# Performance work log

Measured on AMD Instinct MI355X. Metric: run time of the kernel, lower is better.

Reference implementation:

```python
import jax, jax.numpy as jnp
import numpy as np

B, D_IN, D_FEAT, N_EX, N_LAB = 4096, 512, 512, 20000, 100
P_FACTOR = 3.0
EPS = 1e-12  # torch F.normalize eps


def setup_inputs() -> dict:
    key = jax.random.key(0)
    k1, k2, k3, k4 = jax.random.split(key, 4)
    features = jax.random.normal(k1, (B, D_IN), dtype=jnp.float32)
    g_weight = jax.random.normal(k2, (D_FEAT, D_IN), dtype=jnp.float32) * (1.0 / np.sqrt(D_IN))
    ex_features = jax.random.normal(k3, (N_EX, D_IN), dtype=jnp.float32)
    ex_classes = jax.random.uniform(k4, (N_EX, N_LAB), dtype=jnp.float32)
    class_reps = jnp.eye(N_LAB, dtype=jnp.float32)  # one_hot(arange(num_labels)) since class_dim is None
    return {"features": features, "g_weight": g_weight, "ex_features": ex_features,
            "ex_classes": ex_classes, "class_reps": class_reps}


def _l2_normalize(x):
    n = jnp.linalg.norm(x, axis=-1, keepdims=True)
    return x / jnp.maximum(n, EPS)


def _l1_normalize(x):
    n = jnp.sum(jnp.abs(x), axis=-1, keepdims=True)
    return x / jnp.maximum(n, EPS)


def reference(features, g_weight, ex_features, ex_classes, class_reps):
    # g projection (bias-free linear)
    f = features @ g_weight.T          # [B, D_FEAT]
    e = ex_features @ g_weight.T       # [N_EX, D_FEAT]
    # exemplar class representations
    ex_class_reps = _l1_normalize(ex_classes) @ class_reps  # [N_EX, N_LAB]
    # cosine similarity
    s = _l2_normalize(f) @ _l2_normalize(e).T  # [B, N_EX]
    # power-sign activation then L1 row-normalize
    a = jnp.sign(s) * jnp.abs(s) ** P_FACTOR
    a = _l1_normalize(a)
    echo = a @ ex_class_reps           # [B, N_LAB]
    return echo
```

## Files before the change

### kernel.cpp

```cpp
#include <hip/hip_runtime.h>

#define B_ROWS 4096
#define D      512
#define N_EX   20000
#define EXP2   20096
#define N_LAB  100
#define LABP2  128
#define NT2    157
#define SPLITS 16

typedef __attribute__((ext_vector_type(8)))  short short8v;
typedef __attribute__((ext_vector_type(4)))  short short4v;
typedef __attribute__((ext_vector_type(4)))  float f32x4;
typedef __attribute__((ext_vector_type(16))) float f32x16;
typedef __attribute__((ext_vector_type(2)))  int   int2v;
typedef unsigned short u16;

__device__ __forceinline__ u16 f2bf(float x) {
    unsigned u = __builtin_bit_cast(unsigned, x);
    u = u + 0x7FFFu + ((u >> 16) & 1u);
    return (u16)(u >> 16);
}
__device__ __forceinline__ float bf2f(u16 h) {
    unsigned u = ((unsigned)h) << 16;
    return __builtin_bit_cast(float, u);
}

__device__ __forceinline__ float wave_reduce_sum(float v) {
    #pragma unroll
    for (int off = 32; off > 0; off >>= 1) v += __shfl_down(v, off, 64);
    return v;
}

__device__ __forceinline__ void gload16(const void* g, void* l) {
    __builtin_amdgcn_global_load_lds((const __attribute__((address_space(1))) void*)g,
                                     (__attribute__((address_space(3))) void*)l, 16, 0, 0);
}

__device__ __forceinline__ unsigned pk_bf16(float a, float b) {
    unsigned r;
    asm("v_cvt_pk_bf16_f32 %0, %1, %2" : "=v"(r) : "v"(a), "v"(b));
    return r;
}

__device__ __forceinline__ void swap_halves(unsigned &a, unsigned &b) {
#if __has_builtin(__builtin_amdgcn_permlane32_swap)
    int2v r = __builtin_amdgcn_permlane32_swap((int)a, (int)b, false, false);
    a = (unsigned)r[0]; b = (unsigned)r[1];
#else
    unsigned sa = (unsigned)__shfl_xor((int)a, 32, 64);
    unsigned sb = (unsigned)__shfl_xor((int)b, 32, 64);
    if (threadIdx.x & 32) a = sb; else b = sa;
#endif
}

#define MFMA16(a, b, c) __builtin_amdgcn_mfma_f32_16x16x32_bf16((a), (b), (c), 0, 0, 0)
#define MFMA32(a, b, c) __builtin_amdgcn_mfma_f32_32x32x16_bf16((a), (b), (c), 0, 0, 0)

__global__ __launch_bounds__(256, 2)
void proj_k(const float* __restrict__ X, const float* __restrict__ W,
            u16* __restrict__ Chi, int M) {
    __shared__ u16 AH[64][72], AL[64][72], BH[64][72];
    const int tid = threadIdx.x;
    const int lane = tid & 63, wave = tid >> 6;
    const int wm = wave >> 1, wn = wave & 1;
    const int l15 = lane & 15, l4 = lane >> 4;
    const int m0 = blockIdx.x * 64, n0 = blockIdx.y * 64;
    f32x4 acc[2][2] = {};
    for (int kc = 0; kc < 8; ++kc) {
        __syncthreads();
        #pragma unroll
        for (int s = 0; s < 2; ++s) {
            int ix = tid + s * 256;
            int r = ix >> 3, c = ix & 7;
            float va[8] = {0.f,0.f,0.f,0.f,0.f,0.f,0.f,0.f};
            if (m0 + r < M) {
                const float* p = &X[(size_t)(m0 + r) * D + kc * 64 + c * 8];
                float4 t0 = *(const float4*)p, t1 = *(const float4*)(p + 4);
                va[0]=t0.x; va[1]=t0.y; va[2]=t0.z; va[3]=t0.w;
                va[4]=t1.x; va[5]=t1.y; va[6]=t1.z; va[7]=t1.w;
            }
            short8v h, l;
            #pragma unroll
            for (int j = 0; j < 8; ++j) {
                u16 hh = f2bf(va[j]); h[j] = (short)hh; l[j] = (short)f2bf(va[j] - bf2f(hh));
            }
            *(short8v*)&AH[r][c*8] = h; *(short8v*)&AL[r][c*8] = l;
            const float* q = &W[(size_t)(n0 + r) * D + kc * 64 + c * 8];
            float4 s0 = *(const float4*)q, s1 = *(const float4*)(q + 4);
            float vb[8] = {s0.x,s0.y,s0.z,s0.w,s1.x,s1.y,s1.z,s1.w};
            #pragma unroll
            for (int j = 0; j < 8; ++j) h[j] = (short)f2bf(vb[j]);
            *(short8v*)&BH[r][c*8] = h;
        }
        __syncthreads();
        #pragma unroll
        for (int ks = 0; ks < 2; ++ks) {
            const int ko = ks * 32 + l4 * 8;
            short8v ah0 = *(const short8v*)&AH[wm*32      + l15][ko];
            short8v ah1 = *(const short8v*)&AH[wm*32 + 16 + l15][ko];
            short8v al0 = *(const short8v*)&AL[wm*32      + l15][ko];
            short8v al1 = *(const short8v*)&AL[wm*32 + 16 + l15][ko];
            short8v bh0 = *(const short8v*)&BH[wn*32      + l15][ko];
            short8v bh1 = *(const short8v*)&BH[wn*32 + 16 + l15][ko];
            acc[0][0] = MFMA16(ah0, bh0, acc[0][0]); acc[0][0] = MFMA16(al0, bh0, acc[0][0]);
            acc[0][1] = MFMA16(ah0, bh1, acc[0][1]); acc[0][1] = MFMA16(al0, bh1, acc[0][1]);
            acc[1][0] = MFMA16(ah1, bh0, acc[1][0]); acc[1][0] = MFMA16(al1, bh0, acc[1][0]);
            acc[1][1] = MFMA16(ah1, bh1, acc[1][1]); acc[1][1] = MFMA16(al1, bh1, acc[1][1]);
        }
    }
    #pragma unroll
    for (int mi = 0; mi < 2; ++mi)
      #pragma unroll
      for (int ni = 0; ni < 2; ++ni)
        #pragma unroll
        for (int r = 0; r < 4; ++r) {
            int row = m0 + wm*32 + mi*16 + l4*4 + r;
            int col = n0 + wn*32 + ni*16 + l15;
            Chi[(size_t)row * D + col] = f2bf(acc[mi][ni][r]);
        }
}

__global__ __launch_bounds__(128)
void l2norm_k(u16* __restrict__ hi) {
    const int row = blockIdx.x, tid = threadIdx.x;
    const size_t base = (size_t)row * D + tid * 4;
    short4v hv = *(short4v*)&hi[base];
    float v[4]; float ss = 0.f;
    #pragma unroll
    for (int j = 0; j < 4; ++j) { v[j] = bf2f((u16)hv[j]); ss += v[j] * v[j]; }
    ss = wave_reduce_sum(ss);
    __shared__ float red[2];
    if ((tid & 63) == 0) red[tid >> 6] = ss;
    __syncthreads();
    float inv = 1.0f / fmaxf(sqrtf(red[0] + red[1]), 1e-12f);
    short4v ho;
    #pragma unroll
    for (int j = 0; j < 4; ++j) ho[j] = (short)f2bf(v[j] * inv);
    *(short4v*)&hi[base] = ho;
}

__global__ __launch_bounds__(256)
void ecrT_k(const float* __restrict__ exc, const float* __restrict__ creps,
            u16* __restrict__ th) {
    __shared__ float CRT[N_LAB][101];
    __shared__ float EX[128][N_LAB];
    __shared__ float INV[128];
    __shared__ u16 OUT[LABP2][128];
    const int tid = threadIdx.x;
    const int e0 = blockIdx.x * 128;
    for (int i = tid; i < N_LAB * N_LAB; i += 256) {
        int c = i / N_LAB, lab = i % N_LAB;
        CRT[lab][c] = creps[i];
    }
    for (int i = tid; i < 128 * N_LAB; i += 256) {
        int el = i / N_LAB, c = i % N_LAB;
        int e = e0 + el;
        EX[el][c] = (e < N_EX) ? exc[(size_t)e * N_LAB + c] : 0.f;
    }
    __syncthreads();
    if (tid < 128) {
        float s = 0.f;
        for (int c = 0; c < N_LAB; ++c) s += fabsf(EX[tid][c]);
        INV[tid] = 1.0f / fmaxf(s, 1e-12f);
    }
    __syncthreads();
    const int lab = tid & 127;
    for (int el = tid >> 7; el < 128; el += 2) {
        float acc = 0.f;
        if (lab < N_LAB) {
            #pragma unroll 4
            for (int c = 0; c < N_LAB; ++c) acc += EX[el][c] * CRT[lab][c];
            acc *= INV[el];
        }
        OUT[lab][el] = f2bf(acc);
    }
    __syncthreads();
    for (int i = tid; i < LABP2 * 16; i += 256) {
        int lb = i >> 4, ch = i & 15;
        *(short8v*)&th[(size_t)lb * EXP2 + e0 + ch * 8] = *(const short8v*)&OUT[lb][ch * 8];
    }
}

__global__ __launch_bounds__(512, 4)
void fused_k(const u16* __restrict__ fnh, const u16* __restrict__ enh,
             const u16* __restrict__ ecth,
             float* __restrict__ nump, float* __restrict__ denp2) {
    __shared__ u16 SM[2][128][64];
    __shared__ u16 WT[LABP2][128];

    const int tid = threadIdx.x;
    const int l = tid & 63, w = tid >> 6;
    const int we = w >> 2, wq = w & 3;
    const int l31 = l & 31, l5 = l >> 5;
    const int m0 = blockIdx.x * 128;
    const int split = blockIdx.y;
    const int r_in = l >> 3;
    const int c16s = (l & 7) ^ r_in;

    union FragU { short8v s; unsigned u[4]; };

    f32x16 num_acc[4] = {};
    float den_th = 0.f;

    for (int t = split; t < NT2; t += SPLITS) {
        const int e0 = t * 128;
        f32x16 sacc[2] = {};
        for (int kc = 0; kc < 8; ++kc) {
            __syncthreads();
            const int kofs = kc * 64;
            #pragma unroll
            for (int i = 0; i < 2; ++i) {
                const int q = w * 2 + i;
                const int row = q * 8 + r_in;
                gload16(&enh[(size_t)(e0 + row) * D + kofs + c16s * 8],
                        (u16*)&SM[0][0][0] + q * 512);
                gload16(&fnh[(size_t)(m0 + row) * D + kofs + c16s * 8],
                        (u16*)&SM[1][0][0] + q * 512);
            }
            if (kc == 7) {
                #pragma unroll
                for (int p = 0; p < 4; ++p) {
                    const int row = p * 32 + w * 4 + (l >> 4);
                    const int ch = l & 15;
                    gload16(&ecth[(size_t)row * EXP2 + e0 + ((ch ^ (row & 7)) * 8)],
                            &WT[0][0] + (p * 32 + w * 4) * 128);
                }
            }
            __syncthreads();
            #pragma unroll
            for (int ks = 0; ks < 4; ++ks) {
                short8v aE[2], bF;
                #pragma unroll
                for (int ei = 0; ei < 2; ++ei) {
                    int row = we * 64 + ei * 32 + l31;
                    int cc = ((ks * 2 + l5) ^ (row & 7)) * 8;
                    aE[ei] = *(const short8v*)((const u16*)&SM[0][0][0] + row * 64 + cc);
                }
                {
                    int row = wq * 32 + l31;
                    int cc = ((ks * 2 + l5) ^ (row & 7)) * 8;
                    bF = *(const short8v*)((const u16*)&SM[1][0][0] + row * 64 + cc);
                }
                sacc[0] = MFMA32(aE[0], bF, sacc[0]);
                sacc[1] = MFMA32(aE[1], bF, sacc[1]);
            }
        }
        #pragma unroll
        for (int ei = 0; ei < 2; ++ei) {
            float a3[16];
            #pragma unroll
            for (int r = 0; r < 16; ++r) {
                float sv = sacc[ei][r];
                float c3 = sv * sv * sv;
                a3[r] = c3;
                den_th += fabsf(c3);
            }
            FragU fr[2];
            #pragma unroll
            for (int c = 0; c < 2; ++c) {
                unsigned p01 = pk_bf16(a3[c*8+0], a3[c*8+1]);
                unsigned p23 = pk_bf16(a3[c*8+2], a3[c*8+3]);
                unsigned p45 = pk_bf16(a3[c*8+4], a3[c*8+5]);
                unsigned p67 = pk_bf16(a3[c*8+6], a3[c*8+7]);
                swap_halves(p01, p45);
                swap_halves(p23, p67);
                fr[c].u[0] = p01; fr[c].u[1] = p23; fr[c].u[2] = p45; fr[c].u[3] = p67;
            }
            #pragma unroll
            for (int c = 0; c < 2; ++c) {
                const int kch = we * 4 + ei * 2 + c;
                #pragma unroll
                for (int lt = 0; lt < 4; ++lt) {
                    int row = lt * 32 + l31;
                    int cc = ((kch * 2 + l5) ^ (row & 7)) * 8;
                    short8v wf = *(const short8v*)(&WT[0][0] + row * 128 + cc);
                    num_acc[lt] = MFMA32(fr[c].s, wf, num_acc[lt]);
                }
            }
        }
    }

    {
        float v = den_th;
        v += __shfl_xor(v, 32, 64);
        if (l5 == 0)
            denp2[((size_t)split * 2 + we) * B_ROWS + m0 + wq * 32 + l31] = v;
    }

    float* SMf = (float*)&SM[0][0][0];
    __syncthreads();
    #pragma unroll
    for (int half = 0; half < 2; ++half) {
        if (we == 1 && (wq >> 1) == half) {
            #pragma unroll
            for (int lt = 0; lt < 4; ++lt)
                #pragma unroll
                for (int r = 0; r < 16; ++r) {
                    int rowf = (r & 3) + 8 * (r >> 2) + 4 * l5;
                    SMf[((wq & 1) * 32 + rowf) * 128 + lt * 32 + l31] = num_acc[lt][r];
                }
        }
        __syncthreads();
        if (we == 0 && (wq >> 1) == half) {
            #pragma unroll
            for (int lt = 0; lt < 4; ++lt)
                #pragma unroll
                for (int r = 0; r < 16; ++r) {
                    int rowf = (r & 3) + 8 * (r >> 2) + 4 * l5;
                    float v = num_acc[lt][r] + SMf[((wq & 1) * 32 + rowf) * 128 + lt * 32 + l31];
                    int m = m0 + wq * 32 + rowf;
                    nump[((size_t)split * B_ROWS + m) * LABP2 + lt * 32 + l31] = v;
                }
        }
        __syncthreads();
    }
}

__global__ __launch_bounds__(128)
void finalize_k(const float* __restrict__ nump, const float* __restrict__ denp2,
                float* __restrict__ out) {
    const int row = blockIdx.x, tid = threadIdx.x;
    float den = 0.f;
    for (int s = 0; s < 2 * SPLITS; ++s)
        den += denp2[(size_t)s * B_ROWS + row];
    if (tid < N_LAB) {
        float acc = 0.f;
        for (int s = 0; s < SPLITS; ++s)
            acc += nump[((size_t)s * B_ROWS + row) * LABP2 + tid];
        out[(size_t)row * N_LAB + tid] = acc / fmaxf(den, 1e-12f);
    }
}

extern "C" void kernel_launch(void* const* d_in, const int* in_sizes, int n_in,
                              void* d_out, int out_size, void* d_ws, size_t ws_size,
                              hipStream_t stream) {
    (void)in_sizes; (void)n_in; (void)out_size; (void)ws_size;
    const float* features    = (const float*)d_in[0];
    const float* g_weight    = (const float*)d_in[1];
    const float* ex_features = (const float*)d_in[2];
    const float* ex_classes  = (const float*)d_in[3];
    const float* class_reps  = (const float*)d_in[4];
    float* out = (float*)d_out;

    size_t off = 0;
    auto alloc = [&](size_t bytes) {
        void* p = (char*)d_ws + off;
        off += (bytes + 255) & ~(size_t)255;
        return p;
    };
    u16* fnh = (u16*)alloc((size_t)B_ROWS * D * 2);
    u16* enh = (u16*)alloc((size_t)EXP2 * D * 2);
    u16* ecth = (u16*)alloc((size_t)LABP2 * EXP2 * 2);
    float* nump  = (float*)alloc((size_t)SPLITS * B_ROWS * LABP2 * 4);
    float* denp2 = (float*)alloc((size_t)2 * SPLITS * B_ROWS * 4);

    proj_k<<<dim3(B_ROWS / 64, 8), 256, 0, stream>>>(features, g_weight, fnh, B_ROWS);
    proj_k<<<dim3(EXP2 / 64, 8), 256, 0, stream>>>(ex_features, g_weight, enh, N_EX);
    l2norm_k<<<B_ROWS, 128, 0, stream>>>(fnh);
    l2norm_k<<<EXP2, 128, 0, stream>>>(enh);
    ecrT_k<<<NT2, 256, 0, stream>>>(ex_classes, class_reps, ecth);
    fused_k<<<dim3(B_ROWS / 128, SPLITS), 512, 0, stream>>>(fnh, enh, ecth, nump, denp2);
    finalize_k<<<B_ROWS, 128, 0, stream>>>(nump, denp2, out);
}
```

Before: 420.2 us.

## Double-buffer fused similarity kernel and project exemplars via bf16 GEMM

The fused similarity kernel now uses a double-buffered 128x128 LDS tile. It prefetches the next k-chunk, the class-weight tile, or the next tile's first chunk while MFMAs run on the current buffer, which removes one barrier per iteration. The exemplar projection moves from the hi/lo split proj_k path to a plain bf16 conversion followed by a single-pass 128x128 MFMA GEMM, with the nump workspace reused as scratch. This aims to hide global load latency and cut projection cost, at some cost in precision for the exemplar features.

```diff
diff --git a/kernel.cpp b/kernel.cpp
--- a/kernel.cpp
+++ b/kernel.cpp
@@ -56,6 +56,87 @@
 
 #define MFMA16(a, b, c) __builtin_amdgcn_mfma_f32_16x16x32_bf16((a), (b), (c), 0, 0, 0)
 #define MFMA32(a, b, c) __builtin_amdgcn_mfma_f32_32x32x16_bf16((a), (b), (c), 0, 0, 0)
+
+__global__ __launch_bounds__(256)
+void splitH_k(const float* __restrict__ src, u16* __restrict__ dst,
+              int src_rows, int dst_rows) {
+    int i8 = blockIdx.x * 256 + threadIdx.x;
+    if (i8 >= dst_rows * 64) return;
+    int row = i8 >> 6;
+    int e = (i8 & 63) * 8;
+    short8v h = {0,0,0,0,0,0,0,0};
+    if (row < src_rows) {
+        const float* p = &src[(size_t)row * D + e];
+        float4 a = *(const float4*)p, b = *(const float4*)(p + 4);
+        float v[8] = {a.x,a.y,a.z,a.w,b.x,b.y,b.z,b.w};
+        #pragma unroll
+        for (int j = 0; j < 8; ++j) h[j] = (short)f2bf(v[j]);
+    }
+    *(short8v*)&dst[(size_t)row * D + e] = h;
+}
+
+__global__ __launch_bounds__(512, 4)
+void gemm128_k(const u16* __restrict__ A, const u16* __restrict__ B,
+               u16* __restrict__ C) {
+    __shared__ u16 BUF[2][128][128];
+    const int tid = threadIdx.x;
+    const int l = tid & 63, w = tid >> 6;
+    const int wa = w >> 2, wb = w & 3;
+    const int l31 = l & 31, l5 = l >> 5;
+    const int m0 = blockIdx.x * 128, n0 = blockIdx.y * 128;
+    const int qrow_in = l >> 4;
+    const int gs = l & 15;
+
+    f32x16 sacc[2] = {};
+
+    auto STAGE = [&](int nx, int kc_) {
+        const int kofs = kc_ * 64;
+        #pragma unroll
+        for (int i = 0; i < 4; ++i) {
+            const int q = w * 4 + i;
+            const int r = q * 4 + qrow_in;
+            const int g = gs ^ (r & 15);
+            const u16* src = (g < 8)
+                ? &A[(size_t)(m0 + r) * D + kofs + g * 8]
+                : &B[(size_t)(n0 + r) * D + kofs + (g - 8) * 8];
+            gload16(src, (u16*)&BUF[nx][0][0] + q * 512);
+        }
+    };
+
+    STAGE(0, 0);
+    __syncthreads();
+    int cur = 0;
+    for (int kc = 0; kc < 8; ++kc) {
+        if (kc < 7) STAGE(cur ^ 1, kc + 1);
+        const u16* base = &BUF[cur][0][0];
+        #pragma unroll
+        for (int ks = 0; ks < 4; ++ks) {
+            const int gk = ks * 2 + l5;
+            short8v aX[2], bW;
+            #pragma unroll
+            for (int ei = 0; ei < 2; ++ei) {
+                int r = wa * 64 + ei * 32 + l31;
+                aX[ei] = *(const short8v*)(base + r * 128 + (gk ^ (r & 15)) * 8);
+            }
+            {
+                int r = wb * 32 + l31;
+                bW = *(const short8v*)(base + r * 128 + ((gk | 8) ^ (r & 15)) * 8);
+            }
+            sacc[0] = MFMA32(aX[0], bW, sacc[0]);
+            sacc[1] = MFMA32(aX[1], bW, sacc[1]);
+        }
+        __syncthreads();
+        cur ^= 1;
+    }
+    #pragma unroll
+    for (int ei = 0; ei < 2; ++ei)
+        #pragma unroll
+        for (int r = 0; r < 16; ++r) {
+            int row = m0 + wa * 64 + ei * 32 + (r & 3) + 8 * (r >> 2) + 4 * l5;
+            int col = n0 + wb * 32 + l31;
+            C[(size_t)row * D + col] = f2bf(sacc[ei][r]);
+        }
+}
 
 __global__ __launch_bounds__(256, 2)
 void proj_k(const float* __restrict__ X, const float* __restrict__ W,
@@ -186,66 +267,78 @@
 void fused_k(const u16* __restrict__ fnh, const u16* __restrict__ enh,
              const u16* __restrict__ ecth,
              float* __restrict__ nump, float* __restrict__ denp2) {
-    __shared__ u16 SM[2][128][64];
-    __shared__ u16 WT[LABP2][128];
-
+    __shared__ u16 BUF[2][128][128];
     const int tid = threadIdx.x;
     const int l = tid & 63, w = tid >> 6;
     const int we = w >> 2, wq = w & 3;
     const int l31 = l & 31, l5 = l >> 5;
     const int m0 = blockIdx.x * 128;
     const int split = blockIdx.y;
-    const int r_in = l >> 3;
-    const int c16s = (l & 7) ^ r_in;
+    const int qrow_in = l >> 4;
+    const int gs = l & 15;
 
     union FragU { short8v s; unsigned u[4]; };
 
     f32x16 num_acc[4] = {};
     float den_th = 0.f;
 
+    auto STAGE_AB = [&](int nx, int t_, int kc_) {
+        const int e0_ = t_ * 128, kofs = kc_ * 64;
+        #pragma unroll
+        for (int i = 0; i < 4; ++i) {
+            const int q = w * 4 + i;
+            const int r = q * 4 + qrow_in;
+            const int g = gs ^ (r & 15);
+            const u16* src = (g < 8)
+                ? &enh[(size_t)(e0_ + r) * D + kofs + g * 8]
+                : &fnh[(size_t)(m0 + r) * D + kofs + (g - 8) * 8];
+            gload16(src, (u16*)&BUF[nx][0][0] + q * 512);
+        }
+    };
+    auto STAGE_WT = [&](int nx, int t_) {
+        const int e0_ = t_ * 128;
+        #pragma unroll
+        for (int i = 0; i < 4; ++i) {
+            const int q = w * 4 + i;
+            const int lab = q * 4 + qrow_in;
+            const int g = gs ^ (lab & 15);
+            gload16(&ecth[(size_t)lab * EXP2 + e0_ + g * 8],
+                    (u16*)&BUF[nx][0][0] + q * 512);
+        }
+    };
+
+    STAGE_AB(0, split, 0);
+    __syncthreads();
+    int cur = 0;
+
     for (int t = split; t < NT2; t += SPLITS) {
-        const int e0 = t * 128;
         f32x16 sacc[2] = {};
         for (int kc = 0; kc < 8; ++kc) {
-            __syncthreads();
-            const int kofs = kc * 64;
-            #pragma unroll
-            for (int i = 0; i < 2; ++i) {
-                const int q = w * 2 + i;
-                const int row = q * 8 + r_in;
-                gload16(&enh[(size_t)(e0 + row) * D + kofs + c16s * 8],
-                        (u16*)&SM[0][0][0] + q * 512);
-                gload16(&fnh[(size_t)(m0 + row) * D + kofs + c16s * 8],
-                        (u16*)&SM[1][0][0] + q * 512);
-            }
-            if (kc == 7) {
-                #pragma unroll
-                for (int p = 0; p < 4; ++p) {
-                    const int row = p * 32 + w * 4 + (l >> 4);
-                    const int ch = l & 15;
-                    gload16(&ecth[(size_t)row * EXP2 + e0 + ((ch ^ (row & 7)) * 8)],
-                            &WT[0][0] + (p * 32 + w * 4) * 128);
-                }
-            }
-            __syncthreads();
+            if (kc < 7) STAGE_AB(cur ^ 1, t, kc + 1);
+            else        STAGE_WT(cur ^ 1, t);
+            const u16* base = &BUF[cur][0][0];
             #pragma unroll
             for (int ks = 0; ks < 4; ++ks) {
+                const int gk = ks * 2 + l5;
                 short8v aE[2], bF;
                 #pragma unroll
                 for (int ei = 0; ei < 2; ++ei) {
-                    int row = we * 64 + ei * 32 + l31;
-                    int cc = ((ks * 2 + l5) ^ (row & 7)) * 8;
-                    aE[ei] = *(const short8v*)((const u16*)&SM[0][0][0] + row * 64 + cc);
+                    int r = we * 64 + ei * 32 + l31;
+                    aE[ei] = *(const short8v*)(base + r * 128 + (gk ^ (r & 15)) * 8);
                 }
                 {
-                    int row = wq * 32 + l31;
-                    int cc = ((ks * 2 + l5) ^ (row & 7)) * 8;
-                    bF = *(const short8v*)((const u16*)&SM[1][0][0] + row * 64 + cc);
+                    int r = wq * 32 + l31;
+                    bF = *(const short8v*)(base + r * 128 + ((gk | 8) ^ (r & 15)) * 8);
                 }
                 sacc[0] = MFMA32(aE[0], bF, sacc[0]);
                 sacc[1] = MFMA32(aE[1], bF, sacc[1]);
             }
-        }
+            __syncthreads();
+            cur ^= 1;
+        }
+        const int tn = t + SPLITS;
+        if (tn < NT2) STAGE_AB(cur ^ 1, tn, 0);
+        const u16* wbase = &BUF[cur][0][0];
         #pragma unroll
         for (int ei = 0; ei < 2; ++ei) {
             float a3[16];
@@ -269,16 +362,17 @@
             }
             #pragma unroll
             for (int c = 0; c < 2; ++c) {
-                const int kch = we * 4 + ei * 2 + c;
+                const int gw = (we * 4 + ei * 2 + c) * 2 + l5;
                 #pragma unroll
                 for (int lt = 0; lt < 4; ++lt) {
                     int row = lt * 32 + l31;
-                    int cc = ((kch * 2 + l5) ^ (row & 7)) * 8;
-                    short8v wf = *(const short8v*)(&WT[0][0] + row * 128 + cc);
+                    short8v wf = *(const short8v*)(wbase + row * 128 + (gw ^ (row & 15)) * 8);
                     num_acc[lt] = MFMA32(fr[c].s, wf, num_acc[lt]);
                 }
             }
         }
+        __syncthreads();
+        cur ^= 1;
     }
 
     {
@@ -288,7 +382,7 @@
             denp2[((size_t)split * 2 + we) * B_ROWS + m0 + wq * 32 + l31] = v;
     }
 
-    float* SMf = (float*)&SM[0][0][0];
+    float* SMf = (float*)&BUF[0][0][0];
     __syncthreads();
     #pragma unroll
     for (int half = 0; half < 2; ++half) {
@@ -352,11 +446,15 @@
     u16* fnh = (u16*)alloc((size_t)B_ROWS * D * 2);
     u16* enh = (u16*)alloc((size_t)EXP2 * D * 2);
     u16* ecth = (u16*)alloc((size_t)LABP2 * EXP2 * 2);
+    u16* wh  = (u16*)alloc((size_t)D * D * 2);
     float* nump  = (float*)alloc((size_t)SPLITS * B_ROWS * LABP2 * 4);
     float* denp2 = (float*)alloc((size_t)2 * SPLITS * B_ROWS * 4);
-
+    u16* exh = (u16*)nump;
+
+    splitH_k<<<(EXP2 * 64 + 255) / 256, 256, 0, stream>>>(ex_features, exh, N_EX, EXP2);
+    splitH_k<<<(D * 64 + 255) / 256, 256, 0, stream>>>(g_weight, wh, D, D);
+    gemm128_k<<<dim3(EXP2 / 128, 4), 512, 0, stream>>>(exh, wh, enh);
     proj_k<<<dim3(B_ROWS / 64, 8), 256, 0, stream>>>(features, g_weight, fnh, B_ROWS);
-    proj_k<<<dim3(EXP2 / 64, 8), 256, 0, stream>>>(ex_features, g_weight, enh, N_EX);
     l2norm_k<<<B_ROWS, 128, 0, stream>>>(fnh);
     l2norm_k<<<EXP2, 128, 0, stream>>>(enh);
     ecrT_k<<<NT2, 256, 0, stream>>>(ex_classes, class_reps, ecth);
```

New measurement: 432.1 us. +2.8%, slower.
